# Optimization experiments

Hardware: AMD Instinct MI355X
Metric: run time of the kernel (lower is better)

Reference implementation:

```python
import jax, jax.numpy as jnp
import numpy as np

N_NODES = 50000
N_EDGES = 800000
N_GRAPHS = 256
FEAT = 128
HID = 64
HEADS = 4
OUT = 128
NEG_SLOPE = 0.2  # PyG GATConv default leaky_relu slope


def setup_inputs() -> dict:
    key = jax.random.key(0)
    ks = jax.random.split(key, 16)
    x = jax.random.normal(ks[0], (N_NODES, FEAT), dtype=jnp.float32)
    edge_index = jax.random.randint(ks[1], (2, N_EDGES), 0, N_NODES, dtype=jnp.int64)
    batch = jnp.sort(jax.random.randint(ks[2], (N_NODES,), 0, N_GRAPHS, dtype=jnp.int64))
    dims_in = [FEAT, HID * HEADS, HID * HEADS]
    params = {}
    for i, din in enumerate(dims_in):
        s = 1.0 / np.sqrt(din)
        params[f"W{i}"] = jax.random.normal(ks[3 + 4 * i], (din, HEADS * HID), dtype=jnp.float32) * s
        params[f"as{i}"] = jax.random.normal(ks[4 + 4 * i], (HEADS, HID), dtype=jnp.float32) * s
        params[f"ad{i}"] = jax.random.normal(ks[5 + 4 * i], (HEADS, HID), dtype=jnp.float32) * s
        params[f"b{i}"] = jnp.zeros((HEADS * HID,), dtype=jnp.float32)
    params["Wf"] = jax.random.normal(ks[15], (HID * HEADS, OUT), dtype=jnp.float32) / np.sqrt(HID * HEADS)
    params["bf"] = jnp.zeros((OUT,), dtype=jnp.float32)
    return {"x": x, "edge_index": edge_index, "batch": batch, **params}


def _gat_layer(x, src, dst, W, a_s, a_d, b):
    # x: [N, Din] -> h: [N, H, D]
    N = x.shape[0]
    h = (x @ W).reshape(N, HEADS, HID)
    alpha_src = jnp.einsum("nhd,hd->nh", h, a_s)  # [N, H]
    alpha_dst = jnp.einsum("nhd,hd->nh", h, a_d)
    e = jax.nn.leaky_relu(alpha_src[src] + alpha_dst[dst], NEG_SLOPE)  # [E, H]
    # segment softmax over edges sharing the same destination node
    m = jax.ops.segment_max(e, dst, num_segments=N)
    ex = jnp.exp(e - m[dst])
    s = jax.ops.segment_sum(ex, dst, num_segments=N)
    alpha = ex / s[dst]  # [E, H]
    msg = h[src] * alpha[:, :, None]  # [E, H, D]
    out = jax.ops.segment_sum(msg, dst, num_segments=N)  # [N, H, D]
    return out.reshape(N, HEADS * HID) + b


def reference(x, edge_index, batch, W0, as0, ad0, b0, W1, as1, ad1, b1,
              W2, as2, ad2, b2, Wf, bf):
    N = x.shape[0]
    loop = jnp.arange(N, dtype=edge_index.dtype)
    src = jnp.concatenate([edge_index[0], loop])  # PyG GATConv adds self-loops
    dst = jnp.concatenate([edge_index[1], loop])
    for W, a_s, a_d, b in ((W0, as0, ad0, b0), (W1, as1, ad1, b1), (W2, as2, ad2, b2)):
        x = jax.nn.elu(_gat_layer(x, src, dst, W, a_s, a_d, b))
    # global mean pool over graphs
    sums = jax.ops.segment_sum(x, batch, num_segments=N_GRAPHS)  # [G, HID*HEADS]
    cnt = jax.ops.segment_sum(jnp.ones((N,), x.dtype), batch, num_segments=N_GRAPHS)
    g = sums / jnp.maximum(cnt, 1.0)[:, None]
    y = g @ Wf + bf
    norm = jnp.linalg.norm(y, axis=-1, keepdims=True)
    return y / jnp.maximum(norm, 1e-12)
```

## Files before the change

kernel.cpp:

```cpp
#include <hip/hip_runtime.h>
#include <math.h>

#define NND 50000
#define NED 800000
#define ETOT 850000
#define NG 256
#define FEAT 128
#define CCH 256
#define OUTD 128
#define NEG 0.2f
#define NBLK 196
#define M2 50048
#define XBLK 6250

typedef __attribute__((ext_vector_type(8))) _Float16 half8;
typedef __attribute__((ext_vector_type(4))) _Float16 half4;
typedef __attribute__((ext_vector_type(4))) float floatx4;

#if __has_builtin(__builtin_amdgcn_global_load_lds)
#define GLOAD16(g, l) __builtin_amdgcn_global_load_lds( \
    (const __attribute__((address_space(1))) void*)(g), \
    (__attribute__((address_space(3))) void*)(l), 16, 0, 0)
#define HAVE_GLDS 1
#else
#define HAVE_GLDS 0
#endif


__global__ void count_kernel(const int* __restrict__ ei, int* __restrict__ deg) {
    int e = blockIdx.x * 256 + threadIdx.x;
    if (e >= ETOT) return;
    int dst = (e < NED) ? ei[NED + e] : (e - NED);
    atomicAdd(&deg[dst], 1);
}

__global__ __launch_bounds__(256) void scan_part_kernel(const int* __restrict__ deg,
                                                        int* __restrict__ bsum) {
    __shared__ int tile[256];
    int i = blockIdx.x * 256 + threadIdx.x;
    tile[threadIdx.x] = (i < NND) ? deg[i] : 0;
    __syncthreads();
    for (int s = 128; s > 0; s >>= 1) {
        if (threadIdx.x < s) tile[threadIdx.x] += tile[threadIdx.x + s];
        __syncthreads();
    }
    if (threadIdx.x == 0) bsum[blockIdx.x] = tile[0];
}

__global__ __launch_bounds__(256) void scan_write_kernel(const int* __restrict__ deg,
                                                         const int* __restrict__ bsum,
                                                         int* __restrict__ rowptr,
                                                         int* __restrict__ cursor) {
    __shared__ int bs[256];
    __shared__ int tile[256];
    const int t = threadIdx.x, b = blockIdx.x;
    bs[t] = (t < NBLK) ? bsum[t] : 0;
    __syncthreads();
    for (int off = 1; off < 256; off <<= 1) {
        int u = (t >= off) ? bs[t - off] : 0;
        __syncthreads();
        bs[t] += u;
        __syncthreads();
    }
    int boffb = (b == 0) ? 0 : bs[b - 1];
    int total = bs[NBLK - 1];
    int i = b * 256 + t;
    int v = (i < NND) ? deg[i] : 0;
    tile[t] = v;
    __syncthreads();
    for (int off = 1; off < 256; off <<= 1) {
        int u = (t >= off) ? tile[t - off] : 0;
        __syncthreads();
        tile[t] += u;
        __syncthreads();
    }
    if (i < NND) {
        int r = boffb + tile[t] - v;
        rowptr[i] = r;
        cursor[i] = r;
    }
    if (i == 0) rowptr[NND] = total;
}

__global__ void scatter_kernel(const int* __restrict__ ei, int* __restrict__ cursor,
                               int* __restrict__ csrsrc) {
    int e = blockIdx.x * 256 + threadIdx.x;
    if (e >= ETOT) return;
    int s, d;
    if (e < NED) { s = ei[e]; d = ei[NED + e]; } else { s = d = e - NED; }
    int pos = atomicAdd(&cursor[d], 1);
    csrsrc[pos] = s;
}


__global__ __launch_bounds__(256) void prep_kernel(const int* __restrict__ batch,
                                                   int* __restrict__ deg,
                                                   int* __restrict__ gstart,
                                                   const float4* __restrict__ x,
                                                   half4* __restrict__ xo,
                                                   const float* __restrict__ W0,
                                                   const float* __restrict__ W1,
                                                   const float* __restrict__ W2,
                                                   _Float16* __restrict__ wt0,
                                                   _Float16* __restrict__ wt1,
                                                   _Float16* __restrict__ wt2) {
    int b = blockIdx.x;
    if (b < 196) {
        int i = b * 256 + threadIdx.x;
        if (i < NND + 1) deg[i] = 0;
        return;
    }
    b -= 196;
    if (b < 196) {
        int i = b * 256 + threadIdx.x;
        if (i >= NND) return;
        int bb = batch[i];
        int bp = (i == 0) ? -1 : batch[i - 1];
        for (int g = bp + 1; g <= bb; ++g) gstart[g] = i;
        if (i == NND - 1)
            for (int g = bb + 1; g <= NG; ++g) gstart[g] = NND;
        return;
    }
    b -= 196;
    if (b < XBLK) {
        int i = b * 256 + threadIdx.x;
        if (i >= NND * FEAT / 4) return;
        float4 v = x[i];
        half4 o;
        o[0] = (_Float16)v.x; o[1] = (_Float16)v.y;
        o[2] = (_Float16)v.z; o[3] = (_Float16)v.w;
        xo[i] = o;
        return;
    }
    b -= XBLK;
    int j = b * 256 + threadIdx.x;
    if (j < 256 * 128) {
        int n = j >> 7, k = j & 127;
        wt0[j] = (_Float16)W0[k * 256 + n];
        return;
    }
    j -= 256 * 128;
    if (j < 256 * 256) {
        int n = j >> 8, k = j & 255;
        wt1[j] = (_Float16)W1[k * 256 + n];
        return;
    }
    j -= 256 * 256;
    if (j < 256 * 256) {
        int n = j >> 8, k = j & 255;
        wt2[j] = (_Float16)W2[k * 256 + n];
    }
}


#define BK 64

__global__ __launch_bounds__(256, 3) void gemm_mfma_kernel(
        const _Float16* __restrict__ A,
        const _Float16* __restrict__ Bt,
        const float* __restrict__ as_, const float* __restrict__ ad_,
        _Float16* __restrict__ Hm,
        float* __restrict__ asrc, float* __restrict__ adst, int K) {
    __shared__ _Float16 AsF[128 * 64];
    __shared__ _Float16 BsF[128 * 64];
    const int t = threadIdx.x;
    const int bn = blockIdx.x * 128;
    const int bm = blockIdx.y * 128;
    const int lane = t & 63, wv = t >> 6;
    const int wm = (wv >> 1) * 64, wn = (wv & 1) * 64;
    const int fr = lane & 15, q = lane >> 4;

    floatx4 acc[4][4] = {};

    const int lrow = t >> 3;
    const int c8 = t & 7;

    for (int k0 = 0; k0 < K; k0 += BK) {
        for (int p = 0; p < 4; p++) {
            int row = p * 32 + lrow;
            int g8 = c8 ^ (row & 7);
            const _Float16* ga = A + (size_t)(bm + row) * K + k0 + g8 * 8;
            const _Float16* gb = Bt + (size_t)(bn + row) * K + k0 + g8 * 8;
#if HAVE_GLDS
            GLOAD16(ga, &AsF[row * 64 + c8 * 8]);
            GLOAD16(gb, &BsF[row * 64 + c8 * 8]);
#else
            *(half8*)&AsF[row * 64 + c8 * 8] = *(const half8*)ga;
            *(half8*)&BsF[row * 64 + c8 * 8] = *(const half8*)gb;
#endif
        }
        __syncthreads();
        for (int kc = 0; kc < 2; kc++) {
            half8 af[4], bf[4];
            int kb = kc * 4 + q;
            int cs = (kb ^ (fr & 7)) * 8;
            for (int mi = 0; mi < 4; mi++)
                af[mi] = *(const half8*)&AsF[(wm + mi * 16 + fr) * 64 + cs];
            for (int ni = 0; ni < 4; ni++)
                bf[ni] = *(const half8*)&BsF[(wn + ni * 16 + fr) * 64 + cs];
            for (int mi = 0; mi < 4; mi++)
                for (int ni = 0; ni < 4; ni++)
                    acc[mi][ni] = __builtin_amdgcn_mfma_f32_16x16x32_f16(
                        af[mi], bf[ni], acc[mi][ni], 0, 0, 0);
        }
        __syncthreads();
    }

    for (int mi = 0; mi < 4; mi++) {
        int row0 = bm + wm + mi * 16 + q * 4;
        for (int ni = 0; ni < 4; ni++) {
            int col = bn + wn + ni * 16 + fr;
            for (int r = 0; r < 4; r++)
                Hm[(size_t)(row0 + r) * CCH + col] = (_Float16)acc[mi][ni][r];
        }
    }

    const int hd = (bn + wn) >> 6;
    float asf[4], adf[4];
    for (int ni = 0; ni < 4; ni++) {
        asf[ni] = as_[hd * 64 + ni * 16 + fr];
        adf[ni] = ad_[hd * 64 + ni * 16 + fr];
    }
    for (int mi = 0; mi < 4; mi++)
        for (int r = 0; r < 4; r++) {
            float ps = 0.f, pd = 0.f;
            for (int ni = 0; ni < 4; ni++) {
                float v = acc[mi][ni][r];
                ps += v * asf[ni];
                pd += v * adf[ni];
            }
            for (int m = 1; m < 16; m <<= 1) {
                ps += __shfl_xor(ps, m, 64);
                pd += __shfl_xor(pd, m, 64);
            }
            if (fr == 0) {
                int row = bm + wm + mi * 16 + q * 4 + r;
                asrc[row * 4 + hd] = ps;
                adst[row * 4 + hd] = pd;
            }
        }
}


__global__ __launch_bounds__(256) void agg_kernel(const _Float16* __restrict__ H16,
                                                  const float* __restrict__ asrc,
                                                  const float* __restrict__ adst,
                                                  const int* __restrict__ rowptr,
                                                  const int* __restrict__ csrsrc,
                                                  const float4* __restrict__ bias4,
                                                  half8* __restrict__ xo) {
    int wave = threadIdx.x >> 6, lane = threadIdx.x & 63;
    int n = blockIdx.x * 4 + wave;
    if (n >= NND) return;
    int rs = rowptr[n], re = rowptr[n + 1];
    int hd = lane >> 4;
    int sub = lane & 15;
    int l32 = lane & 31;
    int myh = l32 >> 3;
    int epar = lane >> 5;
    float adv = adst[n * 4 + hd];
    float acc[8] = {};
    float ssum = 0.f;
    const char* hbyte = (const char*)H16;
    unsigned loff = (unsigned)l32 * 16u;

    int sl = rs + sub;
    bool ok = sl < re;
    int idx = ok ? csrsrc[sl] : 0;
    unsigned off = (unsigned)idx << 9;
    float aval = asrc[idx * 4 + hd];

    int e0 = rs;
    while (re - e0 >= 16) {
        float a = aval + adv;
        a = fmaxf(a, NEG * a);
        float ev = __expf(a);
        ssum += ev;
        unsigned offcur = off;
        int sl2 = e0 + 16 + sub;
        bool ok2 = sl2 < re;
        int idx2 = ok2 ? csrsrc[sl2] : 0;
        off = (unsigned)idx2 << 9;
        aval = asrc[idx2 * 4 + hd];
        ok = ok2;

        half8 hv[8];
        float wws[8];
        #pragma unroll
        for (int j2 = 0; j2 < 8; j2++) {
            int j = j2 * 2 + epar;
            unsigned o = __shfl(offcur, j, 64);
            wws[j2] = __shfl(ev, myh * 16 + j, 64);
            hv[j2] = *(const half8*)(hbyte + (o + loff));
        }
        #pragma unroll
        for (int j2 = 0; j2 < 8; j2++) {
            float ww = wws[j2];
            #pragma unroll
            for (int k = 0; k < 8; k++)
                acc[k] += ww * (float)hv[j2][k];
        }
        e0 += 16;
    }
    if (e0 < re) {
        float a = aval + adv;
        a = fmaxf(a, NEG * a);
        float ev = ok ? __expf(a) : 0.f;
        ssum += ev;
        int cnt = re - e0;
        #pragma unroll
        for (int j2 = 0; j2 < 8; j2++) {
            if (j2 * 2 >= cnt) break;
            int j = j2 * 2 + epar;
            unsigned o = __shfl(off, j, 64);
            float ww = __shfl(ev, myh * 16 + j, 64);
            half8 hv = *(const half8*)(hbyte + (o + loff));
            #pragma unroll
            for (int k = 0; k < 8; k++)
                acc[k] += ww * (float)hv[k];
        }
    }
    for (int sft = 1; sft < 16; sft <<= 1) ssum += __shfl_xor(ssum, sft, 64);
    float inv = 1.f / __shfl(ssum, myh * 16, 64);
    #pragma unroll
    for (int k = 0; k < 8; k++) acc[k] += __shfl_xor(acc[k], 32, 64);
    if (lane < 32) {
        float4 b0 = bias4[l32 * 2], b1 = bias4[l32 * 2 + 1];
        float o[8];
        o[0] = acc[0] * inv + b0.x; o[1] = acc[1] * inv + b0.y;
        o[2] = acc[2] * inv + b0.z; o[3] = acc[3] * inv + b0.w;
        o[4] = acc[4] * inv + b1.x; o[5] = acc[5] * inv + b1.y;
        o[6] = acc[6] * inv + b1.z; o[7] = acc[7] * inv + b1.w;
        half8 h;
        #pragma unroll
        for (int k = 0; k < 8; k++) {
            float v = o[k];
            v = v > 0.f ? v : expm1f(v);
            h[k] = (_Float16)v;
        }
        xo[(size_t)n * 32 + l32] = h;
    }
}


__global__ __launch_bounds__(256) void poolfinal_kernel(const _Float16* __restrict__ xa,
                                                        const int* __restrict__ gstart,
                                                        const float* __restrict__ Wf,
                                                        const float* __restrict__ bfv,
                                                        float* __restrict__ out) {
    int g = blockIdx.x, t = threadIdx.x;
    __shared__ float gm[256];
    __shared__ float red[128];
    int s = gstart[g], e = gstart[g + 1];
    float acc = 0.f;
    for (int i = s; i < e; i++)
        acc += (float)xa[(size_t)i * CCH + t];
    int cnt = e - s;
    gm[t] = acc / (float)(cnt > 0 ? cnt : 1);
    __syncthreads();
    float a = 0.f;
    if (t < OUTD) {
        a = bfv[t];
        for (int k = 0; k < CCH; k++) a += gm[k] * Wf[k * OUTD + t];
        red[t] = a * a;
    }
    __syncthreads();
    for (int sft = 64; sft > 0; sft >>= 1) {
        if (t < sft) red[t] += red[t + sft];
        __syncthreads();
    }
    if (t < OUTD) out[g * OUTD + t] = a / fmaxf(sqrtf(red[0]), 1e-12f);
}


extern "C" void kernel_launch(void* const* d_in, const int* in_sizes, int n_in,
                              void* d_out, int out_size, void* d_ws, size_t ws_size,
                              hipStream_t stream) {
    const float* x     = (const float*)d_in[0];
    const int*   ei    = (const int*)d_in[1];
    const int*   batch = (const int*)d_in[2];
    const float* W[3]  = {(const float*)d_in[3], (const float*)d_in[7],  (const float*)d_in[11]};
    const float* As[3] = {(const float*)d_in[4], (const float*)d_in[8],  (const float*)d_in[12]};
    const float* Ad[3] = {(const float*)d_in[5], (const float*)d_in[9],  (const float*)d_in[13]};
    const float* Bb[3] = {(const float*)d_in[6], (const float*)d_in[10], (const float*)d_in[14]};
    const float* Wf    = (const float*)d_in[15];
    const float* bf    = (const float*)d_in[16];
    float* out = (float*)d_out;

    _Float16* H16   = (_Float16*)d_ws;
    _Float16* act16 = H16 + (size_t)M2 * CCH;
    _Float16* wt0   = act16 + (size_t)M2 * CCH;
    _Float16* wt1   = wt0 + 256 * 128;
    _Float16* wt2   = wt1 + 256 * 256;
    float* asrc  = (float*)(wt2 + 256 * 256);
    float* adst  = asrc + (size_t)M2 * 4;
    int* deg     = (int*)(adst + (size_t)M2 * 4);
    int* rowptr  = deg + (NND + 1);
    int* cursor  = rowptr + (NND + 1);
    int* csrsrc  = cursor + (NND + 1);
    int* gstart  = csrsrc + ETOT;
    int* bsum    = gstart + (NG + 1);

    _Float16* wt[3] = {wt0, wt1, wt2};

    prep_kernel<<<196 + 196 + XBLK + 640, 256, 0, stream>>>(
        batch, deg, gstart, (const float4*)x, (half4*)act16,
        W[0], W[1], W[2], wt0, wt1, wt2);
    count_kernel<<<(ETOT + 255) / 256, 256, 0, stream>>>(ei, deg);
    scan_part_kernel<<<NBLK, 256, 0, stream>>>(deg, bsum);
    scan_write_kernel<<<NBLK, 256, 0, stream>>>(deg, bsum, rowptr, cursor);
    scatter_kernel<<<(ETOT + 255) / 256, 256, 0, stream>>>(ei, cursor, csrsrc);

    int K = FEAT;
    for (int l = 0; l < 3; l++) {
        dim3 g(2, M2 / 128);
        gemm_mfma_kernel<<<g, 256, 0, stream>>>(act16, wt[l], As[l], Ad[l], H16, asrc, adst, K);
        agg_kernel<<<(NND + 3) / 4, 256, 0, stream>>>(H16, asrc, adst, rowptr, csrsrc,
                                                      (const float4*)Bb[l], (half8*)act16);
        K = CCH;
    }

    poolfinal_kernel<<<NG, 256, 0, stream>>>(act16, gstart, Wf, bf, out);
}
```

Before: 519.4 us.

## Split aggregation per head: one wave per (node, head) with 8-edge parallel gather

The aggregation kernel now assigns each wave a single (node, head) pair instead of a whole node, launching four times as many blocks. Each wave processes 64 edges per iteration, with 8 edge slots of 8 lanes each reading one head's 128-byte slice. The aim is more parallelism and more independent loads in flight for low-degree nodes, and less wasted tail work. In exchange, the index and attention-score loads are repeated for every head, and the final cross-lane reductions get longer.

```diff
diff --git a/kernel.cpp b/kernel.cpp
--- a/kernel.cpp
+++ b/kernel.cpp
@@ -249,83 +249,72 @@
                                                   const int* __restrict__ csrsrc,
                                                   const float4* __restrict__ bias4,
                                                   half8* __restrict__ xo) {
-    int wave = threadIdx.x >> 6, lane = threadIdx.x & 63;
-    int n = blockIdx.x * 4 + wave;
+    const int wave = threadIdx.x >> 6, lane = threadIdx.x & 63;
+    const int b = blockIdx.x;
+    const int g = b & 3;
+    const int n = (b >> 2) * 4 + wave;
     if (n >= NND) return;
-    int rs = rowptr[n], re = rowptr[n + 1];
-    int hd = lane >> 4;
-    int sub = lane & 15;
-    int l32 = lane & 31;
-    int myh = l32 >> 3;
-    int epar = lane >> 5;
-    float adv = adst[n * 4 + hd];
+    const int rs = rowptr[n], re = rowptr[n + 1];
+    const int es = lane >> 3;
+    const int c8 = lane & 7;
+    const float adv = adst[n * 4 + g];
+    const char* hbyte = (const char*)H16;
+    const unsigned loff = (unsigned)(g * 128 + c8 * 16);
     float acc[8] = {};
     float ssum = 0.f;
-    const char* hbyte = (const char*)H16;
-    unsigned loff = (unsigned)l32 * 16u;
-
-    int sl = rs + sub;
+
+    int sl = rs + lane;
     bool ok = sl < re;
     int idx = ok ? csrsrc[sl] : 0;
     unsigned off = (unsigned)idx << 9;
-    float aval = asrc[idx * 4 + hd];
-
-    int e0 = rs;
-    while (re - e0 >= 16) {
-        float a = aval + adv;
-        a = fmaxf(a, NEG * a);
-        float ev = __expf(a);
-        ssum += ev;
-        unsigned offcur = off;
-        int sl2 = e0 + 16 + sub;
-        bool ok2 = sl2 < re;
-        int idx2 = ok2 ? csrsrc[sl2] : 0;
-        off = (unsigned)idx2 << 9;
-        aval = asrc[idx2 * 4 + hd];
-        ok = ok2;
-
-        half8 hv[8];
-        float wws[8];
-        #pragma unroll
-        for (int j2 = 0; j2 < 8; j2++) {
-            int j = j2 * 2 + epar;
-            unsigned o = __shfl(offcur, j, 64);
-            wws[j2] = __shfl(ev, myh * 16 + j, 64);
-            hv[j2] = *(const half8*)(hbyte + (o + loff));
-        }
-        #pragma unroll
-        for (int j2 = 0; j2 < 8; j2++) {
-            float ww = wws[j2];
-            #pragma unroll
-            for (int k = 0; k < 8; k++)
-                acc[k] += ww * (float)hv[j2][k];
-        }
-        e0 += 16;
-    }
-    if (e0 < re) {
+    float aval = asrc[idx * 4 + g];
+
+    for (int e0 = rs; e0 < re; e0 += 64) {
         float a = aval + adv;
         a = fmaxf(a, NEG * a);
         float ev = ok ? __expf(a) : 0.f;
         ssum += ev;
-        int cnt = re - e0;
+        unsigned offcur = off;
+        int sl2 = e0 + 64 + lane;
+        bool ok2 = sl2 < re;
+        int idx2 = ok2 ? csrsrc[sl2] : 0;
+        off = (unsigned)idx2 << 9;
+        aval = asrc[idx2 * 4 + g];
+        ok = ok2;
+
+        int cnt = re - e0; if (cnt > 64) cnt = 64;
+        int nsc = (cnt + 7) >> 3;
+        half8 hv[8];
+        float ws[8];
         #pragma unroll
-        for (int j2 = 0; j2 < 8; j2++) {
-            if (j2 * 2 >= cnt) break;
-            int j = j2 * 2 + epar;
-            unsigned o = __shfl(off, j, 64);
-            float ww = __shfl(ev, myh * 16 + j, 64);
-            half8 hv = *(const half8*)(hbyte + (o + loff));
-            #pragma unroll
-            for (int k = 0; k < 8; k++)
-                acc[k] += ww * (float)hv[k];
-        }
-    }
-    for (int sft = 1; sft < 16; sft <<= 1) ssum += __shfl_xor(ssum, sft, 64);
-    float inv = 1.f / __shfl(ssum, myh * 16, 64);
+        for (int sc = 0; sc < 8; sc++) {
+            if (sc < nsc) {
+                int j = sc * 8 + es;
+                unsigned o = __shfl(offcur, j, 64);
+                ws[sc] = __shfl(ev, j, 64);
+                hv[sc] = *(const half8*)(hbyte + (o + loff));
+            }
+        }
+        #pragma unroll
+        for (int sc = 0; sc < 8; sc++) {
+            if (sc < nsc) {
+                float w = ws[sc];
+                #pragma unroll
+                for (int k = 0; k < 8; k++)
+                    acc[k] += w * (float)hv[sc][k];
+            }
+        }
+    }
+    for (int m = 1; m < 64; m <<= 1) ssum += __shfl_xor(ssum, m, 64);
+    float inv = 1.f / ssum;
     #pragma unroll
-    for (int k = 0; k < 8; k++) acc[k] += __shfl_xor(acc[k], 32, 64);
-    if (lane < 32) {
-        float4 b0 = bias4[l32 * 2], b1 = bias4[l32 * 2 + 1];
+    for (int k = 0; k < 8; k++) {
+        acc[k] += __shfl_xor(acc[k], 8, 64);
+        acc[k] += __shfl_xor(acc[k], 16, 64);
+        acc[k] += __shfl_xor(acc[k], 32, 64);
+    }
+    if (lane < 8) {
+        float4 b0 = bias4[g * 16 + c8 * 2], b1 = bias4[g * 16 + c8 * 2 + 1];
         float o[8];
         o[0] = acc[0] * inv + b0.x; o[1] = acc[1] * inv + b0.y;
         o[2] = acc[2] * inv + b0.z; o[3] = acc[3] * inv + b0.w;
@@ -338,7 +327,7 @@
             v = v > 0.f ? v : expm1f(v);
             h[k] = (_Float16)v;
         }
-        xo[(size_t)n * 32 + l32] = h;
+        xo[(size_t)n * 32 + g * 8 + c8] = h;
     }
 }
 
@@ -415,7 +404,7 @@
     for (int l = 0; l < 3; l++) {
         dim3 g(2, M2 / 128);
         gemm_mfma_kernel<<<g, 256, 0, stream>>>(act16, wt[l], As[l], Ad[l], H16, asrc, adst, K);
-        agg_kernel<<<(NND + 3) / 4, 256, 0, stream>>>(H16, asrc, adst, rowptr, csrsrc,
+        agg_kernel<<<(NND / 4) * 4, 256, 0, stream>>>(H16, asrc, adst, rowptr, csrsrc,
                                                       (const float4*)Bb[l], (half8*)act16);
         K = CCH;
     }
```

Measured after the change: 746.7 us. 43.8% more time.
